# Kernel optimization log

Measured on AMD Instinct MI355X. Metric: run time of the kernel, lower is better.

## Reference

```python
import jax, jax.numpy as jnp
import numpy as np

D_MODEL = 1024


def pos_encoding(seq_len, d_model):
    # pos: [S,1], i: [d/2]
    pos = jnp.arange(seq_len, dtype=jnp.float32)[:, None]
    i = jnp.arange(0, d_model, 2, dtype=jnp.float32)
    angle_rates = 1.0 / jnp.power(10000.0, i / d_model)
    angle_rads = pos * angle_rates  # [S, d/2]
    # NOTE: original concatenates sin block then cos block (not interleaved)
    return jnp.concatenate([jnp.sin(angle_rads), jnp.cos(angle_rads)], axis=-1)  # [S, d]


def setup_inputs() -> dict:
    key = jax.random.key(0)
    ks = jax.random.split(key, 4)
    B, S, D = 4, 2048, D_MODEL
    scale = 1.0 / np.sqrt(D)
    x = jax.random.normal(ks[0], (B, S, D), dtype=jnp.float32)
    Wq = jax.random.normal(ks[1], (D, D), dtype=jnp.float32) * scale
    Wk = jax.random.normal(ks[2], (D, D), dtype=jnp.float32) * scale
    Wv = jax.random.normal(ks[3], (D, D), dtype=jnp.float32) * scale
    bq = jnp.zeros((D,), dtype=jnp.float32)
    bk = jnp.zeros((D,), dtype=jnp.float32)
    bv = jnp.zeros((D,), dtype=jnp.float32)
    return {"x": x, "Wq": Wq, "bq": bq, "Wk": Wk, "bk": bk, "Wv": Wv, "bv": bv}


def reference(x, Wq, bq, Wk, bk, Wv, bv):
    B, S, D = x.shape
    pe = pos_encoding(S, D)  # [S, D]
    h = x + pe[None, :, :]
    q = jnp.einsum('bsd,de->bse', h, Wq) + bq
    k = jnp.einsum('bsd,de->bse', h, Wk) + bk
    v = jnp.einsum('bsd,de->bse', h, Wv) + bv
    logits = jnp.einsum('bqd,bkd->bqk', q, k) / jnp.sqrt(jnp.float32(D))
    attn = jax.nn.softmax(logits, axis=-1)
    out = jnp.einsum('bqk,bkd->bqd', attn, v)
    return x + out
```

## Files before the change

### kernel.cpp

```cpp
#include <hip/hip_runtime.h>
#include <stdint.h>


#define AS1(p) ((__attribute__((address_space(1))) void*)(p))
#define AS3(p) ((__attribute__((address_space(3))) void*)(p))

typedef _Float16 f16x8 __attribute__((ext_vector_type(8)));
typedef _Float16 f16x4 __attribute__((ext_vector_type(4)));
typedef float f32x4 __attribute__((ext_vector_type(4)));

__global__ __launch_bounds__(256) void make_h(const float* __restrict__ x,
                                              _Float16* __restrict__ h) {
  const size_t gid = (size_t)blockIdx.x * 256 + threadIdx.x;
  const size_t e = gid * 4;
  const int d = (int)(e & 1023);
  const int m = (int)(e >> 10);
  const int s = m & 2047;
  const float4 xv = *(const float4*)(x + e);
  const int half = d >> 9;
  const int j0 = d & 511;
  const float c = -0.017988946039016f;
  float p[4];
#pragma unroll
  for (int t = 0; t < 4; t++) {
    const float r = __expf((float)(j0 + t) * c);
    const float a = (float)s * r;
    p[t] = half ? __cosf(a) : __sinf(a);
  }
  f16x4 o;
  o[0] = (_Float16)(xv.x + p[0]);
  o[1] = (_Float16)(xv.y + p[1]);
  o[2] = (_Float16)(xv.z + p[2]);
  o[3] = (_Float16)(xv.w + p[3]);
  *(f16x4*)(h + e) = o;
}

__global__ __launch_bounds__(256) void transpose_w(const float* __restrict__ Wq,
                                                   const float* __restrict__ Wk,
                                                   const float* __restrict__ Wv,
                                                   _Float16* __restrict__ Wt) {
  __shared__ float t[32][33];
  const int z = blockIdx.z;
  const float* W = (z == 0) ? Wq : (z == 1) ? Wk : Wv;
  _Float16* o = Wt + (size_t)z * 1024 * 1024;
  const int tx = threadIdx.x, ty = threadIdx.y;
  const int n0 = blockIdx.x * 32, k0 = blockIdx.y * 32;
#pragma unroll
  for (int i = ty; i < 32; i += 8)
    t[i][tx] = W[(size_t)(k0 + i) * 1024 + (n0 + tx)];
  __syncthreads();
#pragma unroll
  for (int i = ty; i < 32; i += 8)
    o[(size_t)(n0 + i) * 1024 + (k0 + tx)] = (_Float16)t[tx][i];
}

__global__ __launch_bounds__(256) void transpose_v(const _Float16* __restrict__ v,
                                                   _Float16* __restrict__ vT) {
  __shared__ _Float16 t[32][33];
  const int z = blockIdx.z;
  const _Float16* in = v + (size_t)z * 2048 * 1024;
  _Float16* out = vT + (size_t)z * 1024 * 2048;
  const int tx = threadIdx.x, ty = threadIdx.y;
  const int d0 = blockIdx.x * 32, j0 = blockIdx.y * 32;
#pragma unroll
  for (int i = ty; i < 32; i += 8)
    t[i][tx] = in[(size_t)(j0 + i) * 1024 + (d0 + tx)];
  __syncthreads();
#pragma unroll
  for (int i = ty; i < 32; i += 8)
    out[(size_t)(d0 + i) * 2048 + (j0 + tx)] = t[tx][i];
}

__global__ __launch_bounds__(256) void softmax_rows(const float* __restrict__ L,
                                                    _Float16* __restrict__ P) {
  const size_t row = blockIdx.x;
  const float* lr = L + row * 2048;
  _Float16* pr = P + row * 2048;
  const int tid = threadIdx.x;
  const float4 v0 = *(const float4*)(lr + tid * 4);
  const float4 v1 = *(const float4*)(lr + 1024 + tid * 4);
  float mx = fmaxf(fmaxf(fmaxf(v0.x, v0.y), fmaxf(v0.z, v0.w)),
                   fmaxf(fmaxf(v1.x, v1.y), fmaxf(v1.z, v1.w)));
#pragma unroll
  for (int off = 32; off > 0; off >>= 1) mx = fmaxf(mx, __shfl_xor(mx, off));
  __shared__ float redm[4];
  __shared__ float reds[4];
  const int lane = tid & 63, wave = tid >> 6;
  if (lane == 0) redm[wave] = mx;
  __syncthreads();
  mx = fmaxf(fmaxf(redm[0], redm[1]), fmaxf(redm[2], redm[3]));
  float e[8];
  e[0] = __expf(v0.x - mx); e[1] = __expf(v0.y - mx);
  e[2] = __expf(v0.z - mx); e[3] = __expf(v0.w - mx);
  e[4] = __expf(v1.x - mx); e[5] = __expf(v1.y - mx);
  e[6] = __expf(v1.z - mx); e[7] = __expf(v1.w - mx);
  float sm = 0.f;
#pragma unroll
  for (int t = 0; t < 8; t++) sm += e[t];
#pragma unroll
  for (int off = 32; off > 0; off >>= 1) sm += __shfl_xor(sm, off);
  if (lane == 0) reds[wave] = sm;
  __syncthreads();
  sm = reds[0] + reds[1] + reds[2] + reds[3];
  const float inv = 1.0f / sm;
  f16x4 o0, o1;
  o0[0] = (_Float16)(e[0] * inv); o0[1] = (_Float16)(e[1] * inv);
  o0[2] = (_Float16)(e[2] * inv); o0[3] = (_Float16)(e[3] * inv);
  o1[0] = (_Float16)(e[4] * inv); o1[1] = (_Float16)(e[5] * inv);
  o1[2] = (_Float16)(e[6] * inv); o1[3] = (_Float16)(e[7] * inv);
  *(f16x4*)(pr + tid * 4) = o0;
  *(f16x4*)(pr + 1024 + tid * 4) = o1;
}

template <int MODE>
__global__ __launch_bounds__(256) void gemm_bt(
    const _Float16* __restrict__ A0, long long sA,
    const _Float16* __restrict__ B0, long long sB,
    void* __restrict__ C0, long long sC,
    const float* __restrict__ aux0, const float* __restrict__ aux1,
    const float* __restrict__ aux2, long long sX,
    const int K, const int N) {
  __shared__ __align__(16) _Float16 As[128 * 32];
  __shared__ __align__(16) _Float16 Bs[128 * 32];
  const int tid = threadIdx.x;
  const int z = blockIdx.z;
  const int bm0 = blockIdx.x * 128, bn0 = blockIdx.y * 128;
  const _Float16* A = A0 + (size_t)z * sA;
  const _Float16* Bt = B0 + (size_t)z * sB;

  const _Float16* a0 = A + (size_t)(bm0 + (tid >> 2)) * K + (tid & 3) * 8;
  const _Float16* a1 = a0 + (size_t)64 * K;
  const _Float16* b0 = Bt + (size_t)(bn0 + (tid >> 2)) * K + (tid & 3) * 8;
  const _Float16* b1 = b0 + (size_t)64 * K;

  const int lane = tid & 63, wave = tid >> 6;
  const int wr = wave >> 1, wc = wave & 1;
  const int quad = lane >> 4, l16 = lane & 15;

  f32x4 acc[4][4];
#pragma unroll
  for (int i = 0; i < 4; i++)
#pragma unroll
    for (int j = 0; j < 4; j++) {
      f32x4 zz = {0.f, 0.f, 0.f, 0.f};
      acc[i][j] = zz;
    }

  for (int k0 = 0; k0 < K; k0 += 32) {
    __syncthreads();
    __builtin_amdgcn_global_load_lds(AS1(a0 + k0), AS3(&As[tid * 8]), 16, 0, 0);
    __builtin_amdgcn_global_load_lds(AS1(a1 + k0), AS3(&As[tid * 8 + 2048]), 16, 0, 0);
    __builtin_amdgcn_global_load_lds(AS1(b0 + k0), AS3(&Bs[tid * 8]), 16, 0, 0);
    __builtin_amdgcn_global_load_lds(AS1(b1 + k0), AS3(&Bs[tid * 8 + 2048]), 16, 0, 0);
    __syncthreads();
    f16x8 af[4], bfr[4];
#pragma unroll
    for (int i = 0; i < 4; i++)
      af[i] = *(const f16x8*)&As[(wr * 64 + i * 16 + l16) * 32 + quad * 8];
#pragma unroll
    for (int j = 0; j < 4; j++)
      bfr[j] = *(const f16x8*)&Bs[(wc * 64 + j * 16 + l16) * 32 + quad * 8];
#pragma unroll
    for (int i = 0; i < 4; i++)
#pragma unroll
      for (int j = 0; j < 4; j++)
        acc[i][j] = __builtin_amdgcn_mfma_f32_16x16x32_f16(af[i], bfr[j],
                                                           acc[i][j], 0, 0, 0);
  }

  const int rowb = bm0 + wr * 64 + quad * 4;
  const int colb = bn0 + wc * 64 + l16;
  if (MODE == 0) {
    _Float16* C = (_Float16*)C0 + (size_t)z * sC;
    const float* bias = (z == 0) ? aux0 : (z == 1) ? aux1 : aux2;
#pragma unroll
    for (int i = 0; i < 4; i++)
#pragma unroll
      for (int j = 0; j < 4; j++) {
        const int gn = colb + j * 16;
        const float bb = bias[gn];
#pragma unroll
        for (int r = 0; r < 4; r++)
          C[(size_t)(rowb + i * 16 + r) * N + gn] = (_Float16)(acc[i][j][r] + bb);
      }
  } else if (MODE == 1) {
    float* C = (float*)C0 + (size_t)z * sC;
#pragma unroll
    for (int i = 0; i < 4; i++)
#pragma unroll
      for (int j = 0; j < 4; j++)
#pragma unroll
        for (int r = 0; r < 4; r++)
          C[(size_t)(rowb + i * 16 + r) * N + (colb + j * 16)] =
              acc[i][j][r] * 0.03125f;
  } else {
    float* C = (float*)C0 + (size_t)z * sC;
    const float* X = aux0 + (size_t)z * sX;
#pragma unroll
    for (int i = 0; i < 4; i++)
#pragma unroll
      for (int j = 0; j < 4; j++)
#pragma unroll
        for (int r = 0; r < 4; r++) {
          const size_t idx = (size_t)(rowb + i * 16 + r) * N + (colb + j * 16);
          C[idx] = acc[i][j][r] + X[idx];
        }
  }
}

extern "C" void kernel_launch(void* const* d_in, const int* in_sizes, int n_in,
                              void* d_out, int out_size, void* d_ws, size_t ws_size,
                              hipStream_t stream) {
  (void)in_sizes; (void)n_in; (void)out_size; (void)ws_size;
  const float* x  = (const float*)d_in[0];
  const float* Wq = (const float*)d_in[1];
  const float* bq = (const float*)d_in[2];
  const float* Wk = (const float*)d_in[3];
  const float* bk = (const float*)d_in[4];
  const float* Wv = (const float*)d_in[5];
  const float* bv = (const float*)d_in[6];
  float* out = (float*)d_out;
  char* ws = (char*)d_ws;

  _Float16* h      = (_Float16*)(ws);
  _Float16* vT     = (_Float16*)(ws);
  _Float16* Wt     = (_Float16*)(ws + 16777216);
  _Float16* qkv    = (_Float16*)(ws + 23068672);
  _Float16* attn   = (_Float16*)(ws + 23068672);
  float*    logits = (float*)   (ws + 73400320);

  const long long E = 8388608;

  transpose_w<<<dim3(32, 32, 3), dim3(32, 8), 0, stream>>>(Wq, Wk, Wv, Wt);
  make_h<<<8192, 256, 0, stream>>>(x, h);

  gemm_bt<0><<<dim3(64, 8, 3), 256, 0, stream>>>(
      h, 0LL, Wt, 1048576LL, qkv, E, bq, bk, bv, 0LL, 1024, 1024);

  transpose_v<<<dim3(32, 64, 4), dim3(32, 8), 0, stream>>>(qkv + 2 * E, vT);

  gemm_bt<1><<<dim3(16, 16, 4), 256, 0, stream>>>(
      qkv, 2097152LL, qkv + E, 2097152LL, logits, 4194304LL,
      nullptr, nullptr, nullptr, 0LL, 1024, 2048);

  softmax_rows<<<8192, 256, 0, stream>>>(logits, attn);

  gemm_bt<2><<<dim3(16, 8, 4), 256, 0, stream>>>(
      attn, 4194304LL, vT, 2097152LL, out, 2097152LL,
      x, nullptr, nullptr, 2097152LL, 2048, 1024);
}
```

Before: 315.7 us.

## Store logits in fp16 and XOR-swizzle GEMM LDS tiles

The QK^T GEMM now writes scaled logits as fp16 instead of fp32, and softmax reads them as fp16 with 8-wide vector loads and stores. This halves the logits write and read traffic (a 64 MB fp32 buffer). The GEMM also XOR-swizzles the 16-byte column chunk within each LDS row, both when loading from global memory and when reading fragments, to reduce LDS bank conflicts. The cost is reduced logit precision before softmax, which could affect accuracy given the fp16 range.

After: 314.4 us. Within noise of the previous version (-0.4%).

```diff
diff --git a/kernel.cpp b/kernel.cpp
--- a/kernel.cpp
+++ b/kernel.cpp
@@ -71,16 +71,19 @@
     out[(size_t)(d0 + i) * 2048 + (j0 + tx)] = t[tx][i];
 }
 
-__global__ __launch_bounds__(256) void softmax_rows(const float* __restrict__ L,
+__global__ __launch_bounds__(256) void softmax_rows(const _Float16* __restrict__ L,
                                                     _Float16* __restrict__ P) {
   const size_t row = blockIdx.x;
-  const float* lr = L + row * 2048;
+  const _Float16* lr = L + row * 2048;
   _Float16* pr = P + row * 2048;
   const int tid = threadIdx.x;
-  const float4 v0 = *(const float4*)(lr + tid * 4);
-  const float4 v1 = *(const float4*)(lr + 1024 + tid * 4);
-  float mx = fmaxf(fmaxf(fmaxf(v0.x, v0.y), fmaxf(v0.z, v0.w)),
-                   fmaxf(fmaxf(v1.x, v1.y), fmaxf(v1.z, v1.w)));
+  const f16x8 v = *(const f16x8*)(lr + tid * 8);
+  float f[8];
+#pragma unroll
+  for (int t = 0; t < 8; t++) f[t] = (float)v[t];
+  float mx = f[0];
+#pragma unroll
+  for (int t = 1; t < 8; t++) mx = fmaxf(mx, f[t]);
 #pragma unroll
   for (int off = 32; off > 0; off >>= 1) mx = fmaxf(mx, __shfl_xor(mx, off));
   __shared__ float redm[4];
@@ -90,26 +93,19 @@
   __syncthreads();
   mx = fmaxf(fmaxf(redm[0], redm[1]), fmaxf(redm[2], redm[3]));
   float e[8];
-  e[0] = __expf(v0.x - mx); e[1] = __expf(v0.y - mx);
-  e[2] = __expf(v0.z - mx); e[3] = __expf(v0.w - mx);
-  e[4] = __expf(v1.x - mx); e[5] = __expf(v1.y - mx);
-  e[6] = __expf(v1.z - mx); e[7] = __expf(v1.w - mx);
   float sm = 0.f;
 #pragma unroll
-  for (int t = 0; t < 8; t++) sm += e[t];
+  for (int t = 0; t < 8; t++) { e[t] = __expf(f[t] - mx); sm += e[t]; }
 #pragma unroll
   for (int off = 32; off > 0; off >>= 1) sm += __shfl_xor(sm, off);
   if (lane == 0) reds[wave] = sm;
   __syncthreads();
   sm = reds[0] + reds[1] + reds[2] + reds[3];
   const float inv = 1.0f / sm;
-  f16x4 o0, o1;
-  o0[0] = (_Float16)(e[0] * inv); o0[1] = (_Float16)(e[1] * inv);
-  o0[2] = (_Float16)(e[2] * inv); o0[3] = (_Float16)(e[3] * inv);
-  o1[0] = (_Float16)(e[4] * inv); o1[1] = (_Float16)(e[5] * inv);
-  o1[2] = (_Float16)(e[6] * inv); o1[3] = (_Float16)(e[7] * inv);
-  *(f16x4*)(pr + tid * 4) = o0;
-  *(f16x4*)(pr + 1024 + tid * 4) = o1;
+  f16x8 o;
+#pragma unroll
+  for (int t = 0; t < 8; t++) o[t] = (_Float16)(e[t] * inv);
+  *(f16x8*)(pr + tid * 8) = o;
 }
 
 template <int MODE>
@@ -128,14 +124,17 @@
   const _Float16* A = A0 + (size_t)z * sA;
   const _Float16* Bt = B0 + (size_t)z * sB;
 
-  const _Float16* a0 = A + (size_t)(bm0 + (tid >> 2)) * K + (tid & 3) * 8;
+  const int srow = tid >> 2;
+  const int csrc = (tid & 3) ^ ((tid >> 4) & 3);
+  const _Float16* a0 = A + (size_t)(bm0 + srow) * K + csrc * 8;
   const _Float16* a1 = a0 + (size_t)64 * K;
-  const _Float16* b0 = Bt + (size_t)(bn0 + (tid >> 2)) * K + (tid & 3) * 8;
+  const _Float16* b0 = Bt + (size_t)(bn0 + srow) * K + csrc * 8;
   const _Float16* b1 = b0 + (size_t)64 * K;
 
   const int lane = tid & 63, wave = tid >> 6;
   const int wr = wave >> 1, wc = wave & 1;
   const int quad = lane >> 4, l16 = lane & 15;
+  const int cq = (quad ^ ((l16 >> 2) & 3)) * 8;
 
   f32x4 acc[4][4];
 #pragma unroll
@@ -156,10 +155,10 @@
     f16x8 af[4], bfr[4];
 #pragma unroll
     for (int i = 0; i < 4; i++)
-      af[i] = *(const f16x8*)&As[(wr * 64 + i * 16 + l16) * 32 + quad * 8];
+      af[i] = *(const f16x8*)&As[(wr * 64 + i * 16 + l16) * 32 + cq];
 #pragma unroll
     for (int j = 0; j < 4; j++)
-      bfr[j] = *(const f16x8*)&Bs[(wc * 64 + j * 16 + l16) * 32 + quad * 8];
+      bfr[j] = *(const f16x8*)&Bs[(wc * 64 + j * 16 + l16) * 32 + cq];
 #pragma unroll
     for (int i = 0; i < 4; i++)
 #pragma unroll
@@ -170,7 +169,7 @@
 
   const int rowb = bm0 + wr * 64 + quad * 4;
   const int colb = bn0 + wc * 64 + l16;
-  if (MODE == 0) {
+  if (MODE == 0 || MODE == 1) {
     _Float16* C = (_Float16*)C0 + (size_t)z * sC;
     const float* bias = (z == 0) ? aux0 : (z == 1) ? aux1 : aux2;
 #pragma unroll
@@ -178,21 +177,14 @@
 #pragma unroll
       for (int j = 0; j < 4; j++) {
         const int gn = colb + j * 16;
-        const float bb = bias[gn];
-#pragma unroll
-        for (int r = 0; r < 4; r++)
-          C[(size_t)(rowb + i * 16 + r) * N + gn] = (_Float16)(acc[i][j][r] + bb);
+        const float bb = (MODE == 0) ? bias[gn] : 0.f;
+#pragma unroll
+        for (int r = 0; r < 4; r++) {
+          const float val = (MODE == 0) ? (acc[i][j][r] + bb)
+                                        : (acc[i][j][r] * 0.03125f);
+          C[(size_t)(rowb + i * 16 + r) * N + gn] = (_Float16)val;
+        }
       }
-  } else if (MODE == 1) {
-    float* C = (float*)C0 + (size_t)z * sC;
-#pragma unroll
-    for (int i = 0; i < 4; i++)
-#pragma unroll
-      for (int j = 0; j < 4; j++)
-#pragma unroll
-        for (int r = 0; r < 4; r++)
-          C[(size_t)(rowb + i * 16 + r) * N + (colb + j * 16)] =
-              acc[i][j][r] * 0.03125f;
   } else {
     float* C = (float*)C0 + (size_t)z * sC;
     const float* X = aux0 + (size_t)z * sX;
@@ -227,7 +219,7 @@
   _Float16* Wt     = (_Float16*)(ws + 16777216);
   _Float16* qkv    = (_Float16*)(ws + 23068672);
   _Float16* attn   = (_Float16*)(ws + 23068672);
-  float*    logits = (float*)   (ws + 73400320);
+  _Float16* logits = (_Float16*)(ws + 73400320);
 
   const long long E = 8388608;
 
```
